# Kernel tuning notes

Hardware: AMD Instinct MI355X
Metric: run time of the kernel (lower is better)

## Reference

```python
import jax, jax.numpy as jnp
import numpy as np


def conv1x1(x, w, b):
    # x: (b,c,h,w), w: (o,c), b: (o,)
    return jnp.einsum('oc,bchw->bohw', w, x) + b[None, :, None, None]


def make_grid(b, h, w, outH, outW, scale, offset):
    # Replicates the torch grid construction (align_corners=True style normalization).
    gx = ((jnp.arange(outW, dtype=jnp.float32) + 0.5) / scale - 0.5) * 2.0 / (w - 1) - 1.0
    gy = ((jnp.arange(outH, dtype=jnp.float32) + 0.5) / scale - 0.5) * 2.0 / (h - 1) - 1.0
    ix = jnp.broadcast_to(gx[None, None, :], (b, outH, outW))
    iy = jnp.broadcast_to(gy[None, :, None], (b, outH, outW))
    if offset is not None:
        ix = ix + offset[:, 0] * 2.0 / (w - 1)
        iy = iy + offset[:, 1] * 2.0 / (h - 1)
    return ix, iy


def grid_sample_zeros(img, ix, iy):
    # Bilinear grid_sample, padding_mode='zeros', align_corners=False (torch default).
    b, c, h, w = img.shape
    fx = ((ix + 1.0) * w - 1.0) / 2.0
    fy = ((iy + 1.0) * h - 1.0) / 2.0
    x0 = jnp.floor(fx); y0 = jnp.floor(fy)
    x1 = x0 + 1.0; y1 = y0 + 1.0
    wx1 = fx - x0; wx0 = 1.0 - wx1
    wy1 = fy - y0; wy0 = 1.0 - wy1
    bidx = jnp.arange(b)[:, None, None]

    def gather(xc, yc):
        valid = (xc >= 0) & (xc <= w - 1) & (yc >= 0) & (yc <= h - 1)
        xi = jnp.clip(xc, 0, w - 1).astype(jnp.int32)
        yi = jnp.clip(yc, 0, h - 1).astype(jnp.int32)
        v = img[bidx, :, yi, xi]  # (b,H,W,c)
        return jnp.where(valid[..., None], v, 0.0)

    out = (gather(x0, y0) * (wx0 * wy0)[..., None]
           + gather(x1, y0) * (wx1 * wy0)[..., None]
           + gather(x0, y1) * (wx0 * wy1)[..., None]
           + gather(x1, y1) * (wx1 * wy1)[..., None])
    return jnp.transpose(out, (0, 3, 1, 2))  # (b,c,H,W)


def setup_inputs() -> dict:
    key = jax.random.key(0)
    C, E = 64, 4
    ks = jax.random.split(key, 12)
    s = 0.05
    return {
        'x': jax.random.normal(ks[0], (2, C, 128, 128), dtype=jnp.float32),
        'weight_compress': jax.random.normal(ks[1], (E, C // 8, C), dtype=jnp.float32) * s,
        'weight_expand': jax.random.normal(ks[2], (E, C, C // 8), dtype=jnp.float32) * s,
        'w1': jax.random.normal(ks[3], (C, C + 4), dtype=jnp.float32) * s,
        'b1': jax.random.normal(ks[4], (C,), dtype=jnp.float32) * s,
        'w2': jax.random.normal(ks[5], (C, C), dtype=jnp.float32) * s,
        'b2': jax.random.normal(ks[6], (C,), dtype=jnp.float32) * s,
        'wr': jax.random.normal(ks[7], (E, C), dtype=jnp.float32) * s,
        'br': jax.random.normal(ks[8], (E,), dtype=jnp.float32) * s,
        'wo': jax.random.normal(ks[9], (2, C), dtype=jnp.float32) * s,
        'bo': jax.random.normal(ks[10], (2,), dtype=jnp.float32) * s,
        'scale': 2,
        'outH': 256,
        'outW': 256,
    }


def reference(x, weight_compress, weight_expand, w1, b1, w2, b2, wr, br, wo, bo, scale, outH, outW):
    b, c, h, w = x.shape
    # relative sub-pixel coordinates
    ah = jnp.arange(outH, dtype=jnp.float32)
    aw = jnp.arange(outW, dtype=jnp.float32)
    coor_h = (ah + 0.5) / scale - jnp.floor((ah + 0.5) / scale + 0.001) - 0.5  # (outH,)
    coor_w = (aw + 0.5) / scale - jnp.floor((aw + 0.5) / scale + 0.001) - 0.5  # (outW,)
    ones_hw = jnp.full((outH, outW), 1.0 / scale, dtype=jnp.float32)
    coords = jnp.stack([ones_hw, ones_hw,
                        jnp.broadcast_to(coor_h[:, None], (outH, outW)),
                        jnp.broadcast_to(coor_w[None, :], (outH, outW))], axis=0)  # (4,H,W)
    coords = jnp.broadcast_to(coords[None], (b, 4, outH, outW))

    ix, iy = make_grid(b, h, w, outH, outW, scale, None)
    pre_fea = grid_sample_zeros(x, ix, iy)  # (b,C,H,W)

    inp = jnp.concatenate([coords, pre_fea], axis=1)  # (b,C+4,H,W)
    emb = jax.nn.relu(conv1x1(jax.nn.relu(conv1x1(inp, w1, b1)), w2, b2))

    offset = conv1x1(emb, wo, bo)  # (b,2,H,W)
    ix2, iy2 = make_grid(b, h, w, outH, outW, scale, offset)
    fea0 = grid_sample_zeros(x, ix2, iy2)  # (b,C,H,W)

    r = jax.nn.sigmoid(conv1x1(emb, wr, br))  # (b,E,H,W) routing weights
    # per-pixel expert-blended compress->expand (algebraically identical to
    # materializing per-pixel weight matrices, but as E small GEMM pairs)
    comp = jnp.einsum('behw,edc,bchw->bdhw', r, weight_compress, fea0)  # (b,C/8,H,W)
    out = jnp.einsum('behw,ecd,bdhw->bchw', r, weight_expand, comp)    # (b,C,H,W)
    return out + fea0
```

## Files before the change

kernel.cpp:

```cpp
#include <hip/hip_runtime.h>
#include <math.h>

#define BATCH 2
#define C 64
#define HIN 128
#define WIN 128
#define HW (HIN * WIN)
#define OH 256
#define OW 256

#define BLK 256
#define PIX 64
#define SC 16
#define ASTR 72
#define YHSTR 17
#define YSTR 33
#define OSTR 68

#define WS_W2  4096
#define WS_WC  8192
#define WS_WE  10240
#define WS_WH  12288
#define WS_TOT 13312


typedef __attribute__((ext_vector_type(8))) short bf16x8;
typedef __attribute__((ext_vector_type(4))) float f32x4;

__device__ __forceinline__ unsigned short f2bf(float f) {
    unsigned u = __float_as_uint(f);
    u += 0x7FFFu + ((u >> 16) & 1u);
    return (unsigned short)(u >> 16);
}

__device__ __forceinline__ void bilin_setup(float gx, float gy,
    int& i00, int& i10, int& i01, int& i11,
    float& w00, float& w10, float& w01, float& w11)
{
    const float fx = ((gx + 1.0f) * WIN - 1.0f) * 0.5f;
    const float fy = ((gy + 1.0f) * HIN - 1.0f) * 0.5f;
    const float x0 = floorf(fx), y0 = floorf(fy);
    const float wx1 = fx - x0, wx0 = 1.0f - wx1;
    const float wy1 = fy - y0, wy0 = 1.0f - wy1;
    const float x1 = x0 + 1.0f, y1 = y0 + 1.0f;
    const bool vx0 = (x0 >= 0.0f) && (x0 <= (float)(WIN - 1));
    const bool vx1 = (x1 >= 0.0f) && (x1 <= (float)(WIN - 1));
    const bool vy0 = (y0 >= 0.0f) && (y0 <= (float)(HIN - 1));
    const bool vy1 = (y1 >= 0.0f) && (y1 <= (float)(HIN - 1));
    const int xi0 = (int)fminf(fmaxf(x0, 0.0f), (float)(WIN - 1));
    const int xi1 = (int)fminf(fmaxf(x1, 0.0f), (float)(WIN - 1));
    const int yi0 = (int)fminf(fmaxf(y0, 0.0f), (float)(HIN - 1));
    const int yi1 = (int)fminf(fmaxf(y1, 0.0f), (float)(HIN - 1));
    w00 = wx0 * wy0 * ((vx0 && vy0) ? 1.0f : 0.0f);
    w10 = wx1 * wy0 * ((vx1 && vy0) ? 1.0f : 0.0f);
    w01 = wx0 * wy1 * ((vx0 && vy1) ? 1.0f : 0.0f);
    w11 = wx1 * wy1 * ((vx1 && vy1) ? 1.0f : 0.0f);
    i00 = yi0 * WIN + xi0;  i10 = yi0 * WIN + xi1;
    i01 = yi1 * WIN + xi0;  i11 = yi1 * WIN + xi1;
}

__global__ __launch_bounds__(256) void prep_kernel(
    const float* __restrict__ wcm, const float* __restrict__ wex,
    const float* __restrict__ w1,  const float* __restrict__ w2,
    const float* __restrict__ wr,  const float* __restrict__ wo,
    unsigned short* __restrict__ wsb)
{
    const int i = blockIdx.x * 256 + threadIdx.x;
    if (i >= WS_TOT) return;
    float v = 0.0f;
    if (i < WS_W2) {
        const int n = i >> 6, k = i & 63;
        v = w1[n * (C + 4) + 4 + k];
    } else if (i < WS_WC) {
        v = w2[i - WS_W2];
    } else if (i < WS_WE) {
        v = wcm[i - WS_WC];
    } else if (i < WS_WH) {
        v = wex[i - WS_WE];
    } else {
        const int j = i - WS_WH;
        const int n = j >> 6, k = j & 63;
        v = (n < 2) ? wo[n * C + k] : ((n < 6) ? wr[(n - 2) * C + k] : 0.0f);
    }
    wsb[i] = f2bf(v);
}

__global__ __launch_bounds__(BLK, 4) void scab_kernel(
    const float* __restrict__ x,
    const float* __restrict__ w1,
    const float* __restrict__ b1,
    const float* __restrict__ b2,
    const float* __restrict__ br,
    const float* __restrict__ bo,
    const unsigned short* __restrict__ wsb,
    float* __restrict__ out)
{
    __shared__ __align__(16) short act[PIX * ASTR];
    __shared__ __align__(16) float red[PIX * OSTR];

    const int tid  = threadIdx.x;
    const int lane = tid & 63;
    const int s    = __builtin_amdgcn_readfirstlane(tid >> 6);
    const int cb   = s * SC;
    const int l15  = lane & 15;
    const int quad = lane >> 4;
    const int nn   = cb + l15;

    const int gp = blockIdx.x * PIX + lane;
    const int ox = gp & (OW - 1);
    const int oy = (gp >> 8) & (OH - 1);
    const int bb = gp >> 16;

    const float gx = ((ox + 0.5f) * 0.5f - 0.5f) * (2.0f / (WIN - 1)) - 1.0f;
    const float gy = ((oy + 0.5f) * 0.5f - 0.5f) * (2.0f / (HIN - 1)) - 1.0f;

    const float* __restrict__ xb = x + bb * (C * HW);

    const int nt1  = s & 1;
    const int eo_g = nt1 * 16 + l15;
    bf16x8 bw1[2], bw2[2], bwc[2], bhd[2], bwe;
    #pragma unroll
    for (int ks = 0; ks < 2; ++ks) {
        bw1[ks] = *(const bf16x8*)(wsb +         nn   * 64 + ks * 32 + quad * 8);
        bw2[ks] = *(const bf16x8*)(wsb + WS_W2 + nn   * 64 + ks * 32 + quad * 8);
        bwc[ks] = *(const bf16x8*)(wsb + WS_WC + eo_g * 64 + ks * 32 + quad * 8);
        bhd[ks] = *(const bf16x8*)(wsb + WS_WH + l15  * 64 + ks * 32 + quad * 8);
    }
    bwe = *(const bf16x8*)(wsb + WS_WE + (quad * C + nn) * 8);

    {
        int i00, i10, i01, i11;
        float w00, w10, w01, w11;
        bilin_setup(gx, gy, i00, i10, i01, i11, w00, w10, w01, w11);
        bf16x8 v0, v1;
        #pragma unroll
        for (int kk = 0; kk < SC; kk += 4) {
            float l[16];
            #pragma unroll
            for (int k = 0; k < 4; ++k) {
                const float* __restrict__ xc = xb + (cb + kk + k) * HW;
                l[4*k+0] = xc[i00]; l[4*k+1] = xc[i10];
                l[4*k+2] = xc[i01]; l[4*k+3] = xc[i11];
            }
            #pragma unroll
            for (int k = 0; k < 4; ++k) {
                const float pf = l[4*k]*w00 + l[4*k+1]*w10 + l[4*k+2]*w01 + l[4*k+3]*w11;
                const short b = (short)f2bf(pf);
                if (kk + k < 8) v0[kk + k] = b; else v1[kk + k - 8] = b;
            }
        }
        *(bf16x8*)&act[lane * ASTR + cb]     = v0;
        *(bf16x8*)&act[lane * ASTR + cb + 8] = v1;
    }
    __syncthreads();

    const float coor_h = (oy & 1) ? 0.25f : -0.25f;
    f32x4 acc[4];
    {
        const float4 wh = *(const float4*)(w1 + nn * (C + 4));
        const float qn = b1[nn] + (wh.x + wh.y) * 0.5f + wh.z * coor_h;
        const float e0 = qn - 0.25f * wh.w;
        const float e1 = qn + 0.25f * wh.w;
        #pragma unroll
        for (int t = 0; t < 4; ++t) acc[t] = (f32x4){e0, e1, e0, e1};
    }
    #pragma unroll
    for (int t = 0; t < 4; ++t) {
        #pragma unroll
        for (int ks = 0; ks < 2; ++ks) {
            const bf16x8 af = *(const bf16x8*)&act[(t*16 + l15) * ASTR + ks*32 + quad*8];
            acc[t] = __builtin_amdgcn_mfma_f32_16x16x32_bf16(af, bw1[ks], acc[t], 0, 0, 0);
        }
    }
    __syncthreads();
    #pragma unroll
    for (int t = 0; t < 4; ++t)
        #pragma unroll
        for (int r = 0; r < 4; ++r)
            act[(t*16 + quad*4 + r) * ASTR + nn] = (short)f2bf(fmaxf(acc[t][r], 0.0f));
    __syncthreads();

    {
        const float b2n = b2[nn];
        #pragma unroll
        for (int t = 0; t < 4; ++t) acc[t] = (f32x4){b2n, b2n, b2n, b2n};
    }
    #pragma unroll
    for (int t = 0; t < 4; ++t) {
        #pragma unroll
        for (int ks = 0; ks < 2; ++ks) {
            const bf16x8 af = *(const bf16x8*)&act[(t*16 + l15) * ASTR + ks*32 + quad*8];
            acc[t] = __builtin_amdgcn_mfma_f32_16x16x32_bf16(af, bw2[ks], acc[t], 0, 0, 0);
        }
    }
    __syncthreads();
    #pragma unroll
    for (int t = 0; t < 4; ++t)
        #pragma unroll
        for (int r = 0; r < 4; ++r)
            act[(t*16 + quad*4 + r) * ASTR + nn] = (short)f2bf(fmaxf(acc[t][r], 0.0f));
    __syncthreads();

    {
        f32x4 yac = (f32x4){0.0f, 0.0f, 0.0f, 0.0f};
        #pragma unroll
        for (int ks = 0; ks < 2; ++ks) {
            const bf16x8 af = *(const bf16x8*)&act[(s*16 + l15) * ASTR + ks*32 + quad*8];
            yac = __builtin_amdgcn_mfma_f32_16x16x32_bf16(af, bhd[ks], yac, 0, 0, 0);
        }
        #pragma unroll
        for (int r = 0; r < 4; ++r)
            red[(s*16 + quad*4 + r) * YHSTR + l15] = yac[r];
    }
    __syncthreads();

    const float* __restrict__ yp = &red[lane * YHSTR];
    const float offx = bo[0] + yp[0];
    const float offy = bo[1] + yp[1];
    const float rg0 = 1.0f / (1.0f + __expf(-(br[0] + yp[2])));
    const float rg1 = 1.0f / (1.0f + __expf(-(br[1] + yp[3])));
    const float rg2 = 1.0f / (1.0f + __expf(-(br[2] + yp[4])));
    const float rg3 = 1.0f / (1.0f + __expf(-(br[3] + yp[5])));

    float f[SC];
    {
        int j00, j10, j01, j11;
        float v00, v10, v01, v11;
        bilin_setup(gx + offx * (2.0f / (WIN - 1)),
                    gy + offy * (2.0f / (HIN - 1)),
                    j00, j10, j01, j11, v00, v10, v01, v11);
        bf16x8 v0, v1;
        #pragma unroll
        for (int kk = 0; kk < SC; kk += 4) {
            float l[16];
            #pragma unroll
            for (int k = 0; k < 4; ++k) {
                const float* __restrict__ xc = xb + (cb + kk + k) * HW;
                l[4*k+0] = xc[j00]; l[4*k+1] = xc[j10];
                l[4*k+2] = xc[j01]; l[4*k+3] = xc[j11];
            }
            #pragma unroll
            for (int k = 0; k < 4; ++k) {
                const float fc = l[4*k]*v00 + l[4*k+1]*v10 + l[4*k+2]*v01 + l[4*k+3]*v11;
                f[kk + k] = fc;
                const short b = (short)f2bf(fc);
                if (kk + k < 8) v0[kk + k] = b; else v1[kk + k - 8] = b;
            }
        }
        *(bf16x8*)&act[lane * ASTR + cb]     = v0;
        *(bf16x8*)&act[lane * ASTR + cb + 8] = v1;
    }
    __syncthreads();

    {
        const int mb = (s >> 1) * 2;
        #pragma unroll
        for (int mi = 0; mi < 2; ++mi) {
            const int mt = mb + mi;
            f32x4 yac = (f32x4){0.0f, 0.0f, 0.0f, 0.0f};
            #pragma unroll
            for (int ks = 0; ks < 2; ++ks) {
                const bf16x8 af = *(const bf16x8*)&act[(mt*16 + l15) * ASTR + ks*32 + quad*8];
                yac = __builtin_amdgcn_mfma_f32_16x16x32_bf16(af, bwc[ks], yac, 0, 0, 0);
            }
            #pragma unroll
            for (int r = 0; r < 4; ++r)
                red[(mt*16 + quad*4 + r) * YSTR + nt1*16 + l15] = yac[r];
        }
    }
    __syncthreads();

    {
        float comp[8];
        const float* __restrict__ yr = &red[lane * YSTR];
        #pragma unroll
        for (int d = 0; d < 8; ++d) {
            float v = rg0 * yr[d];
            v = fmaf(rg1, yr[8 + d],  v);
            v = fmaf(rg2, yr[16 + d], v);
            v = fmaf(rg3, yr[24 + d], v);
            comp[d] = v;
        }
        bf16x8 t0, t1;
        #pragma unroll
        for (int d = 0; d < 8; ++d) {
            t0[d] = (short)f2bf(rg0 * comp[d]);
            t1[d] = (short)f2bf(rg1 * comp[d]);
        }
        bf16x8 t2, t3;
        #pragma unroll
        for (int d = 0; d < 8; ++d) {
            t2[d] = (short)f2bf(rg2 * comp[d]);
            t3[d] = (short)f2bf(rg3 * comp[d]);
        }
        *(bf16x8*)&act[lane * ASTR + 0]  = t0;
        *(bf16x8*)&act[lane * ASTR + 8]  = t1;
        *(bf16x8*)&act[lane * ASTR + 16] = t2;
        *(bf16x8*)&act[lane * ASTR + 24] = t3;
    }
    __syncthreads();

    #pragma unroll
    for (int t = 0; t < 4; ++t) {
        f32x4 oac = (f32x4){0.0f, 0.0f, 0.0f, 0.0f};
        const bf16x8 af = *(const bf16x8*)&act[(t*16 + l15) * ASTR + quad*8];
        oac = __builtin_amdgcn_mfma_f32_16x16x32_bf16(af, bwe, oac, 0, 0, 0);
        #pragma unroll
        for (int r = 0; r < 4; ++r)
            red[(t*16 + quad*4 + r) * OSTR + nn] = oac[r];
    }
    __syncthreads();

    float* __restrict__ ob = out + bb * (C * OH * OW) + oy * OW + ox;
    const float* __restrict__ orow = &red[lane * OSTR + cb];
    #pragma unroll
    for (int kk = 0; kk < SC; kk += 4) {
        const float4 e4 = *(const float4*)(orow + kk);
        ob[(cb + kk + 0) * (OH * OW)] = f[kk + 0] + e4.x;
        ob[(cb + kk + 1) * (OH * OW)] = f[kk + 1] + e4.y;
        ob[(cb + kk + 2) * (OH * OW)] = f[kk + 2] + e4.z;
        ob[(cb + kk + 3) * (OH * OW)] = f[kk + 3] + e4.w;
    }
}

extern "C" void kernel_launch(void* const* d_in, const int* in_sizes, int n_in,
                              void* d_out, int out_size, void* d_ws, size_t ws_size,
                              hipStream_t stream) {
    const float* x   = (const float*)d_in[0];
    const float* wcm = (const float*)d_in[1];
    const float* wex = (const float*)d_in[2];
    const float* w1  = (const float*)d_in[3];
    const float* b1  = (const float*)d_in[4];
    const float* w2  = (const float*)d_in[5];
    const float* b2  = (const float*)d_in[6];
    const float* wr  = (const float*)d_in[7];
    const float* br  = (const float*)d_in[8];
    const float* wo  = (const float*)d_in[9];
    const float* bo  = (const float*)d_in[10];
    float* out = (float*)d_out;
    unsigned short* wsb = (unsigned short*)d_ws;

    prep_kernel<<<(WS_TOT + 255) / 256, 256, 0, stream>>>(wcm, wex, w1, w2, wr, wo, wsb);

    const int total  = BATCH * OH * OW;
    const int blocks = total / PIX;
    scab_kernel<<<blocks, BLK, 0, stream>>>(x, w1, b1, b2, br, bo, wsb, out);
}
```

Before: 117.3 us.

## Stage first-pass bilinear source tile in LDS via global_load_lds, ping-pong activation buffers

Each block's 64 output pixels share one output row, so their first grid-sample only touches two input rows and 34 columns per channel. The block now loads that tile for all 64 channels into shared memory with direct global-to-LDS loads, and interpolates from LDS. This replaces four scattered global gathers per channel per pixel. The second change aliases a second activation buffer onto the reduction buffer so successive MLP layers ping-pong, removing two barriers. The cost is more aliasing of shared memory, which depends on barrier placement being correct.

Result: slower. 120.3 us (+2.5%).

```diff
diff --git a/kernel.cpp b/kernel.cpp
--- a/kernel.cpp
+++ b/kernel.cpp
@@ -16,6 +16,7 @@
 #define YHSTR 17
 #define YSTR 33
 #define OSTR 68
+#define TCOLS 34
 
 #define WS_W2  4096
 #define WS_WC  8192
@@ -31,6 +32,12 @@
     unsigned u = __float_as_uint(f);
     u += 0x7FFFu + ((u >> 16) & 1u);
     return (unsigned short)(u >> 16);
+}
+
+__device__ __forceinline__ void gld_lds4(const float* g, float* l) {
+    __builtin_amdgcn_global_load_lds(
+        (const __attribute__((address_space(1))) void*)g,
+        (__attribute__((address_space(3))) void*)l, 4, 0, 0);
 }
 
 __device__ __forceinline__ void bilin_setup(float gx, float gy,
@@ -97,6 +104,8 @@
 {
     __shared__ __align__(16) short act[PIX * ASTR];
     __shared__ __align__(16) float red[PIX * OSTR];
+    float* const xt  = red;
+    short* const act2 = (short*)red;
 
     const int tid  = threadIdx.x;
     const int lane = tid & 63;
@@ -116,6 +125,25 @@
 
     const float* __restrict__ xb = x + bb * (C * HW);
 
+    const float fy  = ((gy + 1.0f) * HIN - 1.0f) * 0.5f;
+    const float y0f = floorf(fy);
+    const int yi0 = (int)fminf(fmaxf(y0f, 0.0f), (float)(HIN - 1));
+    const int yi1 = (int)fminf(fmaxf(y0f + 1.0f, 0.0f), (float)(HIN - 1));
+    const int ox0 = ox & ~63;
+    const float gx0 = ((ox0 + 0.5f) * 0.5f - 0.5f) * (2.0f / (WIN - 1)) - 1.0f;
+    const float fx0 = ((gx0 + 1.0f) * WIN - 1.0f) * 0.5f;
+    const int g0 = (int)floorf(fx0);
+
+    #pragma unroll
+    for (int t = 0; t < 17; ++t) {
+        const int idx = t * 256 + tid;
+        const int rc  = (int)(((unsigned)idx * 61681u) >> 21);
+        const int col = idx - rc * 34;
+        const int gc  = min(max(g0 + col, 0), WIN - 1);
+        const int yr  = (rc & 1) ? yi1 : yi0;
+        gld_lds4(xb + (rc >> 1) * HW + yr * WIN + gc, &xt[idx]);
+    }
+
     const int nt1  = s & 1;
     const int eo_g = nt1 * 16 + l15;
     bf16x8 bw1[2], bw2[2], bwc[2], bhd[2], bwe;
@@ -128,26 +156,32 @@
     }
     bwe = *(const bf16x8*)(wsb + WS_WE + (quad * C + nn) * 8);
 
-    {
-        int i00, i10, i01, i11;
-        float w00, w10, w01, w11;
-        bilin_setup(gx, gy, i00, i10, i01, i11, w00, w10, w01, w11);
+    const float fx  = ((gx + 1.0f) * WIN - 1.0f) * 0.5f;
+    const float x0f = floorf(fx);
+    const float wx1 = fx - x0f, wx0 = 1.0f - wx1;
+    const float wy1 = fy - y0f, wy0 = 1.0f - wy1;
+    const bool vx0 = (x0f >= 0.0f) && (x0f <= (float)(WIN - 1));
+    const bool vx1 = (x0f + 1.0f >= 0.0f) && (x0f + 1.0f <= (float)(WIN - 1));
+    const bool vy0 = (y0f >= 0.0f) && (y0f <= (float)(HIN - 1));
+    const bool vy1 = (y0f + 1.0f >= 0.0f) && (y0f + 1.0f <= (float)(HIN - 1));
+    const float w00 = wx0 * wy0 * ((vx0 && vy0) ? 1.0f : 0.0f);
+    const float w10 = wx1 * wy0 * ((vx1 && vy0) ? 1.0f : 0.0f);
+    const float w01 = wx0 * wy1 * ((vx0 && vy1) ? 1.0f : 0.0f);
+    const float w11 = wx1 * wy1 * ((vx1 && vy1) ? 1.0f : 0.0f);
+    const int lx0 = (int)fminf(fmaxf(x0f, 0.0f), (float)(WIN - 1)) - g0;
+    const int lx1 = (int)fminf(fmaxf(x0f + 1.0f, 0.0f), (float)(WIN - 1)) - g0;
+
+    __syncthreads();
+
+    {
         bf16x8 v0, v1;
         #pragma unroll
-        for (int kk = 0; kk < SC; kk += 4) {
-            float l[16];
-            #pragma unroll
-            for (int k = 0; k < 4; ++k) {
-                const float* __restrict__ xc = xb + (cb + kk + k) * HW;
-                l[4*k+0] = xc[i00]; l[4*k+1] = xc[i10];
-                l[4*k+2] = xc[i01]; l[4*k+3] = xc[i11];
-            }
-            #pragma unroll
-            for (int k = 0; k < 4; ++k) {
-                const float pf = l[4*k]*w00 + l[4*k+1]*w10 + l[4*k+2]*w01 + l[4*k+3]*w11;
-                const short b = (short)f2bf(pf);
-                if (kk + k < 8) v0[kk + k] = b; else v1[kk + k - 8] = b;
-            }
+        for (int kk = 0; kk < SC; ++kk) {
+            const float* T = xt + (cb + kk) * (2 * TCOLS);
+            const float pf = T[lx0] * w00 + T[lx1] * w10
+                           + T[TCOLS + lx0] * w01 + T[TCOLS + lx1] * w11;
+            const short b = (short)f2bf(pf);
+            if (kk < 8) v0[kk] = b; else v1[kk - 8] = b;
         }
         *(bf16x8*)&act[lane * ASTR + cb]     = v0;
         *(bf16x8*)&act[lane * ASTR + cb + 8] = v1;
@@ -172,12 +206,11 @@
             acc[t] = __builtin_amdgcn_mfma_f32_16x16x32_bf16(af, bw1[ks], acc[t], 0, 0, 0);
         }
     }
-    __syncthreads();
     #pragma unroll
     for (int t = 0; t < 4; ++t)
         #pragma unroll
         for (int r = 0; r < 4; ++r)
-            act[(t*16 + quad*4 + r) * ASTR + nn] = (short)f2bf(fmaxf(acc[t][r], 0.0f));
+            act2[(t*16 + quad*4 + r) * ASTR + nn] = (short)f2bf(fmaxf(acc[t][r], 0.0f));
     __syncthreads();
 
     {
@@ -189,11 +222,10 @@
     for (int t = 0; t < 4; ++t) {
         #pragma unroll
         for (int ks = 0; ks < 2; ++ks) {
-            const bf16x8 af = *(const bf16x8*)&act[(t*16 + l15) * ASTR + ks*32 + quad*8];
+            const bf16x8 af = *(const bf16x8*)&act2[(t*16 + l15) * ASTR + ks*32 + quad*8];
             acc[t] = __builtin_amdgcn_mfma_f32_16x16x32_bf16(af, bw2[ks], acc[t], 0, 0, 0);
         }
     }
-    __syncthreads();
     #pragma unroll
     for (int t = 0; t < 4; ++t)
         #pragma unroll
```

## Use paired float2 bilinear gathers, packed bf16 converts, and ping-pong LDS buffers

Applied to the files above, without the earlier changes.

Bilinear sampling now loads two adjacent texels per row as a float2, with the horizontal weights remapped onto a clamped base column. This halves the number of gather instructions per channel. Float-to-bf16 conversion switches from the manual rounding sequence to the hardware v_cvt_pk_bf16_f32 packed instruction. The MLP layers ping-pong between the act buffer and the reused red buffer, which removes two __syncthreads barriers. The float2 loads may be misaligned for odd base columns, and the weight remapping adds a little selection arithmetic.

Result: no change. 118.7 us (+1.2%).

```diff
diff --git a/kernel.cpp b/kernel.cpp
--- a/kernel.cpp
+++ b/kernel.cpp
@@ -26,6 +26,7 @@
 
 typedef __attribute__((ext_vector_type(8))) short bf16x8;
 typedef __attribute__((ext_vector_type(4))) float f32x4;
+typedef __attribute__((ext_vector_type(4))) unsigned u32x4;
 
 __device__ __forceinline__ unsigned short f2bf(float f) {
     unsigned u = __float_as_uint(f);
@@ -33,30 +34,40 @@
     return (unsigned short)(u >> 16);
 }
 
-__device__ __forceinline__ void bilin_setup(float gx, float gy,
-    int& i00, int& i10, int& i01, int& i11,
-    float& w00, float& w10, float& w01, float& w11)
+__device__ __forceinline__ unsigned cvtpk(float lo, float hi) {
+    unsigned r;
+    asm("v_cvt_pk_bf16_f32 %0, %1, %2" : "=v"(r) : "v"(lo), "v"(hi));
+    return r;
+}
+
+__device__ __forceinline__ void bilin_pair(float gx, float gy,
+    int& p0, int& p1, float& u0, float& u1, float& t0, float& t1)
 {
     const float fx = ((gx + 1.0f) * WIN - 1.0f) * 0.5f;
     const float fy = ((gy + 1.0f) * HIN - 1.0f) * 0.5f;
     const float x0 = floorf(fx), y0 = floorf(fy);
     const float wx1 = fx - x0, wx0 = 1.0f - wx1;
     const float wy1 = fy - y0, wy0 = 1.0f - wy1;
-    const float x1 = x0 + 1.0f, y1 = y0 + 1.0f;
     const bool vx0 = (x0 >= 0.0f) && (x0 <= (float)(WIN - 1));
-    const bool vx1 = (x1 >= 0.0f) && (x1 <= (float)(WIN - 1));
+    const bool vx1 = (x0 + 1.0f >= 0.0f) && (x0 + 1.0f <= (float)(WIN - 1));
     const bool vy0 = (y0 >= 0.0f) && (y0 <= (float)(HIN - 1));
-    const bool vy1 = (y1 >= 0.0f) && (y1 <= (float)(HIN - 1));
+    const bool vy1 = (y0 + 1.0f >= 0.0f) && (y0 + 1.0f <= (float)(HIN - 1));
+    const float w00 = wx0 * wy0 * ((vx0 && vy0) ? 1.0f : 0.0f);
+    const float w10 = wx1 * wy0 * ((vx1 && vy0) ? 1.0f : 0.0f);
+    const float w01 = wx0 * wy1 * ((vx0 && vy1) ? 1.0f : 0.0f);
+    const float w11 = wx1 * wy1 * ((vx1 && vy1) ? 1.0f : 0.0f);
     const int xi0 = (int)fminf(fmaxf(x0, 0.0f), (float)(WIN - 1));
-    const int xi1 = (int)fminf(fmaxf(x1, 0.0f), (float)(WIN - 1));
+    const int xi1 = (int)fminf(fmaxf(x0 + 1.0f, 0.0f), (float)(WIN - 1));
     const int yi0 = (int)fminf(fmaxf(y0, 0.0f), (float)(HIN - 1));
-    const int yi1 = (int)fminf(fmaxf(y1, 0.0f), (float)(HIN - 1));
-    w00 = wx0 * wy0 * ((vx0 && vy0) ? 1.0f : 0.0f);
-    w10 = wx1 * wy0 * ((vx1 && vy0) ? 1.0f : 0.0f);
-    w01 = wx0 * wy1 * ((vx0 && vy1) ? 1.0f : 0.0f);
-    w11 = wx1 * wy1 * ((vx1 && vy1) ? 1.0f : 0.0f);
-    i00 = yi0 * WIN + xi0;  i10 = yi0 * WIN + xi1;
-    i01 = yi1 * WIN + xi0;  i11 = yi1 * WIN + xi1;
+    const int yi1 = (int)fminf(fmaxf(y0 + 1.0f, 0.0f), (float)(HIN - 1));
+    const int bx = min(xi0, WIN - 2);
+    const int s0 = xi0 - bx, s1 = xi1 - bx;
+    u0 = (s0 ? 0.0f : w00) + (s1 ? 0.0f : w10);
+    u1 = (s0 ? w00 : 0.0f) + (s1 ? w10 : 0.0f);
+    t0 = (s0 ? 0.0f : w01) + (s1 ? 0.0f : w11);
+    t1 = (s0 ? w01 : 0.0f) + (s1 ? w11 : 0.0f);
+    p0 = yi0 * WIN + bx;
+    p1 = yi1 * WIN + bx;
 }
 
 __global__ __launch_bounds__(256) void prep_kernel(
@@ -97,6 +108,7 @@
 {
     __shared__ __align__(16) short act[PIX * ASTR];
     __shared__ __align__(16) float red[PIX * OSTR];
+    short* const act2 = (short*)red;
 
     const int tid  = threadIdx.x;
     const int lane = tid & 63;
@@ -129,28 +141,32 @@
     bwe = *(const bf16x8*)(wsb + WS_WE + (quad * C + nn) * 8);
 
     {
-        int i00, i10, i01, i11;
-        float w00, w10, w01, w11;
-        bilin_setup(gx, gy, i00, i10, i01, i11, w00, w10, w01, w11);
-        bf16x8 v0, v1;
-        #pragma unroll
-        for (int kk = 0; kk < SC; kk += 4) {
-            float l[16];
-            #pragma unroll
-            for (int k = 0; k < 4; ++k) {
-                const float* __restrict__ xc = xb + (cb + kk + k) * HW;
-                l[4*k+0] = xc[i00]; l[4*k+1] = xc[i10];
-                l[4*k+2] = xc[i01]; l[4*k+3] = xc[i11];
+        int p0, p1;
+        float u0, u1, t0, t1;
+        bilin_pair(gx, gy, p0, p1, u0, u1, t0, t1);
+        float pf[SC];
+        #pragma unroll
+        for (int kb = 0; kb < SC; kb += 8) {
+            float2 a[8], b[8];
+            #pragma unroll
+            for (int k = 0; k < 8; ++k) {
+                const float* __restrict__ xc = xb + (cb + kb + k) * HW;
+                a[k] = *(const float2*)(xc + p0);
+                b[k] = *(const float2*)(xc + p1);
             }
             #pragma unroll
-            for (int k = 0; k < 4; ++k) {
-                const float pf = l[4*k]*w00 + l[4*k+1]*w10 + l[4*k+2]*w01 + l[4*k+3]*w11;
-                const short b = (short)f2bf(pf);
-                if (kk + k < 8) v0[kk + k] = b; else v1[kk + k - 8] = b;
-            }
-        }
-        *(bf16x8*)&act[lane * ASTR + cb]     = v0;
-        *(bf16x8*)&act[lane * ASTR + cb + 8] = v1;
+            for (int k = 0; k < 8; ++k)
+                pf[kb + k] = fmaf(a[k].x, u0, fmaf(a[k].y, u1,
+                             fmaf(b[k].x, t0, b[k].y * t1)));
+        }
+        u32x4 v0, v1;
+        #pragma unroll
+        for (int d = 0; d < 4; ++d) {
+            v0[d] = cvtpk(pf[2*d],     pf[2*d + 1]);
+            v1[d] = cvtpk(pf[8 + 2*d], pf[8 + 2*d + 1]);
+        }
+        *(u32x4*)&act[lane * ASTR + cb]     = v0;
+        *(u32x4*)&act[lane * ASTR + cb + 8] = v1;
     }
     __syncthreads();
 
@@ -172,12 +188,15 @@
             acc[t] = __builtin_amdgcn_mfma_f32_16x16x32_bf16(af, bw1[ks], acc[t], 0, 0, 0);
         }
     }
-    __syncthreads();
-    #pragma unroll
-    for (int t = 0; t < 4; ++t)
-        #pragma unroll
-        for (int r = 0; r < 4; ++r)
-            act[(t*16 + quad*4 + r) * ASTR + nn] = (short)f2bf(fmaxf(acc[t][r], 0.0f));
+    #pragma unroll
+    for (int t = 0; t < 4; ++t) {
+        const unsigned p01 = cvtpk(fmaxf(acc[t][0], 0.0f), fmaxf(acc[t][1], 0.0f));
+        const unsigned p23 = cvtpk(fmaxf(acc[t][2], 0.0f), fmaxf(acc[t][3], 0.0f));
+        act2[(t*16 + quad*4 + 0) * ASTR + nn] = (short)(p01 & 0xffffu);
+        act2[(t*16 + quad*4 + 1) * ASTR + nn] = (short)(p01 >> 16);
+        act2[(t*16 + quad*4 + 2) * ASTR + nn] = (short)(p23 & 0xffffu);
+        act2[(t*16 + quad*4 + 3) * ASTR + nn] = (short)(p23 >> 16);
+    }
     __syncthreads();
 
     {
@@ -189,16 +208,19 @@
     for (int t = 0; t < 4; ++t) {
         #pragma unroll
         for (int ks = 0; ks < 2; ++ks) {
-            const bf16x8 af = *(const bf16x8*)&act[(t*16 + l15) * ASTR + ks*32 + quad*8];
+            const bf16x8 af = *(const bf16x8*)&act2[(t*16 + l15) * ASTR + ks*32 + quad*8];
             acc[t] = __builtin_amdgcn_mfma_f32_16x16x32_bf16(af, bw2[ks], acc[t], 0, 0, 0);
         }
     }
-    __syncthreads();
-    #pragma unroll
-    for (int t = 0; t < 4; ++t)
-        #pragma unroll
-        for (int r = 0; r < 4; ++r)
-            act[(t*16 + quad*4 + r) * ASTR + nn] = (short)f2bf(fmaxf(acc[t][r], 0.0f));
+    #pragma unroll
+    for (int t = 0; t < 4; ++t) {
+        const unsigned p01 = cvtpk(fmaxf(acc[t][0], 0.0f), fmaxf(acc[t][1], 0.0f));
+        const unsigned p23 = cvtpk(fmaxf(acc[t][2], 0.0f), fmaxf(acc[t][3], 0.0f));
+        act[(t*16 + quad*4 + 0) * ASTR + nn] = (short)(p01 & 0xffffu);
+        act[(t*16 + quad*4 + 1) * ASTR + nn] = (short)(p01 >> 16);
+        act[(t*16 + quad*4 + 2) * ASTR + nn] = (short)(p23 & 0xffffu);
+        act[(t*16 + quad*4 + 3) * ASTR + nn] = (short)(p23 >> 16);
+    }
     __syncthreads();
 
     {
@@ -224,31 +246,33 @@
 
     float f[SC];
     {
-        int j00, j10, j01, j11;
-        float v00, v10, v01, v11;
-        bilin_setup(gx + offx * (2.0f / (WIN - 1)),
-                    gy + offy * (2.0f / (HIN - 1)),
-                    j00, j10, j01, j11, v00, v10, v01, v11);
-        bf16x8 v0, v1;
-        #pragma unroll
-        for (int kk = 0; kk < SC; kk += 4) {
-            float l[16];
-            #pragma unroll
-            for (int k = 0; k < 4; ++k) {
-                const float* __restrict__ xc = xb + (cb + kk + k) * HW;
-                l[4*k+0] = xc[j00]; l[4*k+1] = xc[j10];
-                l[4*k+2] = xc[j01]; l[4*k+3] = xc[j11];
+        int p0, p1;
+        float u0, u1, t0, t1;
+        bilin_pair(gx + offx * (2.0f / (WIN - 1)),
+                   gy + offy * (2.0f / (HIN - 1)),
+                   p0, p1, u0, u1, t0, t1);
+        #pragma unroll
+        for (int kb = 0; kb < SC; kb += 8) {
+            float2 a[8], b[8];
+            #pragma unroll
+            for (int k = 0; k < 8; ++k) {
+                const float* __restrict__ xc = xb + (cb + kb + k) * HW;
+                a[k] = *(const float2*)(xc + p0);
+                b[k] = *(const float2*)(xc + p1);
             }
             #pragma unroll
-            for (int k = 0; k < 4; ++k) {
-                const float fc = l[4*k]*v00 + l[4*k+1]*v10 + l[4*k+2]*v01 + l[4*k+3]*v11;
-                f[kk + k] = fc;
-                const short b = (short)f2bf(fc);
-                if (kk + k < 8) v0[kk + k] = b; else v1[kk + k - 8] = b;
-            }
-        }
-        *(bf16x8*)&act[lane * ASTR + cb]     = v0;
-        *(bf16x8*)&act[lane * ASTR + cb + 8] = v1;
+            for (int k = 0; k < 8; ++k)
+                f[kb + k] = fmaf(a[k].x, u0, fmaf(a[k].y, u1,
+                            fmaf(b[k].x, t0, b[k].y * t1)));
+        }
+        u32x4 v0, v1;
+        #pragma unroll
+        for (int d = 0; d < 4; ++d) {
+            v0[d] = cvtpk(f[2*d],     f[2*d + 1]);
+            v1[d] = cvtpk(f[8 + 2*d], f[8 + 2*d + 1]);
+        }
+        *(u32x4*)&act[lane * ASTR + cb]     = v0;
+        *(u32x4*)&act[lane * ASTR + cb + 8] = v1;
     }
     __syncthreads();
 
@@ -281,22 +305,18 @@
             v = fmaf(rg3, yr[24 + d], v);
             comp[d] = v;
         }
-        bf16x8 t0, t1;
-        #pragma unroll
-        for (int d = 0; d < 8; ++d) {
-            t0[d] = (short)f2bf(rg0 * comp[d]);
-            t1[d] = (short)f2bf(rg1 * comp[d]);
-        }
-        bf16x8 t2, t3;
-        #pragma unroll
-        for (int d = 0; d < 8; ++d) {
-            t2[d] = (short)f2bf(rg2 * comp[d]);
-            t3[d] = (short)f2bf(rg3 * comp[d]);
-        }
-        *(bf16x8*)&act[lane * ASTR + 0]  = t0;
-        *(bf16x8*)&act[lane * ASTR + 8]  = t1;
-        *(bf16x8*)&act[lane * ASTR + 16] = t2;
-        *(bf16x8*)&act[lane * ASTR + 24] = t3;
+        u32x4 T0, T1, T2, T3;
+        #pragma unroll
+        for (int d = 0; d < 4; ++d) {
+            T0[d] = cvtpk(rg0 * comp[2*d], rg0 * comp[2*d + 1]);
+            T1[d] = cvtpk(rg1 * comp[2*d], rg1 * comp[2*d + 1]);
+            T2[d] = cvtpk(rg2 * comp[2*d], rg2 * comp[2*d + 1]);
+            T3[d] = cvtpk(rg3 * comp[2*d], rg3 * comp[2*d + 1]);
+        }
+        *(u32x4*)&act[lane * ASTR + 0]  = T0;
+        *(u32x4*)&act[lane * ASTR + 8]  = T1;
+        *(u32x4*)&act[lane * ASTR + 16] = T2;
+        *(u32x4*)&act[lane * ASTR + 24] = T3;
     }
     __syncthreads();
 
```
